# Optimization experiments

Hardware: AMD Instinct MI355X
Metric: run time of the kernel (lower is better)

## Reference

```python
import jax, jax.numpy as jnp
import numpy as np

B, LQ, LK, D, H = 8, 512, 512, 512, 128

def setup_inputs() -> dict:
    key = jax.random.key(0)
    k1, k2, k3, k4, k5 = jax.random.split(key, 5)
    qs = jax.random.normal(k1, (B, LQ, D), dtype=jnp.float32)
    ks = jax.random.normal(k2, (B, LK, D), dtype=jnp.float32)
    # Dense kernels: flax Dense stores kernel as [in_features, out_features]
    Wq = jax.random.normal(k3, (D, H), dtype=jnp.float32) / np.sqrt(D)
    Wk = jax.random.normal(k4, (D, H), dtype=jnp.float32) / np.sqrt(D)
    wv = jax.random.normal(k5, (H,), dtype=jnp.float32) / np.sqrt(H)
    return {"qs": qs, "ks": ks, "Wq": Wq, "Wk": Wk, "wv": wv}

def reference(qs, ks, Wq, Wk, wv):
    # Project queries and keys into the shared hidden space: [B,Lq,H], [B,Lk,H]
    q = jnp.einsum("bqd,dh->bqh", qs, Wq)
    k = jnp.einsum("bkd,dh->bkh", ks, Wk)
    # Broadcast-add -> tanh -> linear reduce over H: scores [B,Lq,Lk]
    feats = jnp.tanh(q[:, :, None, :] + k[:, None, :, :])  # [B,Lq,Lk,H]
    return jnp.einsum("bqkh,h->bqk", feats, wv)
```

## Files before the change

kernel.cpp:

```cpp
#include <hip/hip_runtime.h>
#include <hip/hip_bf16.h>
#include <cstdint>

#define B_   8
#define LQ_  512
#define LK_  512
#define D_   512
#define H_   128

typedef __attribute__((ext_vector_type(8))) short  short8;
typedef __attribute__((ext_vector_type(4))) float  float4v;

#define TANH_C 2.8853900817779268f

__device__ __forceinline__ short bf16rne(float x) {
  uint32_t u = __float_as_uint(x);
  return (short)((u + 0x7fffu + ((u >> 16) & 1u)) >> 16);
}

__device__ __forceinline__ float4v splat4(float x) {
  return (float4v){x, x, x, x};
}

__global__ __launch_bounds__(256) void prep_kernel(
    const float* __restrict__ Wq, const float* __restrict__ Wk,
    const float* __restrict__ wv,
    short* __restrict__ WqF, short* __restrict__ WkF,
    float* __restrict__ w2, float* __restrict__ W0buf) {
  int g = blockIdx.x * 256 + threadIdx.x;
  if (blockIdx.x == 0) {
    int t = threadIdx.x;
    if (t < H_) w2[t] = -2.0f * wv[t];
    if (t == H_) {
      float s = 0.f;
      for (int h = 0; h < H_; ++h) s += wv[h];
      W0buf[0] = s;
    }
  }
  int m = g >> 13;
  int r = g & 8191;
  int l  = r & 63;
  int kb = (r >> 6) & 15;
  int nt = r >> 10;
  int col = nt * 16 + (l & 15);
  int k0  = kb * 32 + ((l >> 4) << 3);
  const float* W = m ? Wk : Wq;
  short8 f;
#pragma unroll
  for (int j = 0; j < 8; ++j) f[j] = bf16rne(W[(k0 + j) * H_ + col]);
  ((short8*)(m ? WkF : WqF))[r] = f;
}

__global__ __launch_bounds__(256) void proj_kernel(
    const float* __restrict__ qs, const float* __restrict__ ks,
    const short* __restrict__ WqF, const short* __restrict__ WkF,
    float* __restrict__ qp, float* __restrict__ kp) {
  int blk  = blockIdx.x;
  int wave = threadIdx.x >> 6;
  int l    = threadIdx.x & 63;
  int grow = blk * 16;
  int m    = (grow >= 4096) ? 1 : 0;
  int r0   = grow - (m ? 4096 : 0);
  const float*  A  = m ? ks : qs;
  const short8* BF = (const short8*)(m ? WkF : WqF);
  float* out = m ? kp : qp;

  float4v acc[2];
  acc[0] = (float4v){0.f, 0.f, 0.f, 0.f};
  acc[1] = (float4v){0.f, 0.f, 0.f, 0.f};

  int quad = l >> 4;
  int arow = r0 + (l & 15);
  const float* aptr = A + (size_t)arow * D_ + quad * 8;
  int t0 = wave * 2;

#pragma unroll 4
  for (int kb = 0; kb < 16; ++kb) {
    float4v a0 = *(const float4v*)(aptr + kb * 32);
    float4v a1 = *(const float4v*)(aptr + kb * 32 + 4);
    short8 af;
#pragma unroll
    for (int j = 0; j < 4; ++j) { af[j] = bf16rne(a0[j]); af[j + 4] = bf16rne(a1[j]); }
#pragma unroll
    for (int tt = 0; tt < 2; ++tt) {
      short8 bf = BF[((t0 + tt) * 16 + kb) * 64 + l];
      acc[tt] = __builtin_amdgcn_mfma_f32_16x16x32_bf16(af, bf, acc[tt], 0, 0, 0);
    }
  }

#pragma unroll
  for (int tt = 0; tt < 2; ++tt)
#pragma unroll
    for (int r = 0; r < 4; ++r) {
      int row = r0 + quad * 4 + r;
      int col = (t0 + tt) * 16 + (l & 15);
      out[(size_t)row * H_ + col] = __builtin_amdgcn_exp2f(acc[tt][r] * TANH_C);
    }
}

__global__ __launch_bounds__(128, 2) void score_kernel(
    const float* __restrict__ qp, const float* __restrict__ kp,
    const float* __restrict__ w2, const float* __restrict__ W0buf,
    float* __restrict__ out) {
  __shared__ float qt[64 * 68];
  __shared__ float kt[64 * 36];
  __shared__ float wl[H_];

  int b = blockIdx.z, qtile = blockIdx.y, ktile = blockIdx.x;
  int t = threadIdx.x;
  int tx = t & 7, ty = t >> 3;

  const float* qbase = qp + (size_t)(b * LQ_ + qtile * 64) * H_;
  const float* kbase = kp + (size_t)(b * LK_ + ktile * 32) * H_;

  float W0 = W0buf[0];

  if (t < 32) *(float4v*)&wl[t * 4] = *(const float4v*)&w2[t * 4];

  float4v acc[4];
  const float4v ones = (float4v){1.f, 1.f, 1.f, 1.f};
#pragma unroll
  for (int i = 0; i < 4; ++i) acc[i] = (float4v){0.f, 0.f, 0.f, 0.f};

  int lr = t >> 4, lc = t & 15;

  for (int hc = 0; hc < 2; ++hc) {
    __syncthreads();
#pragma unroll
    for (int s = 0; s < 8; ++s) {
      int row = lr + 8 * s;
      *(float4v*)&qt[row * 68 + lc * 4] =
          *(const float4v*)&qbase[row * H_ + hc * 64 + lc * 4];
    }
#pragma unroll
    for (int s = 0; s < 4; ++s) {
      int row = lr + 8 * s;
      float4v g = *(const float4v*)&kbase[row * H_ + hc * 64 + lc * 4];
#pragma unroll
      for (int u = 0; u < 4; ++u) kt[(lc * 4 + u) * 36 + row] = g[u];
    }
    __syncthreads();

#pragma unroll 4
    for (int h0 = 0; h0 < 64; h0 += 4) {
      float4v kv[4];
#pragma unroll
      for (int hh = 0; hh < 4; ++hh)
        kv[hh] = *(const float4v*)&kt[(h0 + hh) * 36 + tx * 4];
      float4v w4 = *(const float4v*)&wl[hc * 64 + h0];

#pragma unroll
      for (int i = 0; i < 4; ++i) {
        float4v qv = *(const float4v*)&qt[(ty + 16 * i) * 68 + h0];
        float4v den0 = __builtin_elementwise_fma(splat4(qv[0]), kv[0], ones);
        float4v den1 = __builtin_elementwise_fma(splat4(qv[1]), kv[1], ones);
        float4v den2 = __builtin_elementwise_fma(splat4(qv[2]), kv[2], ones);
        float4v den3 = __builtin_elementwise_fma(splat4(qv[3]), kv[3], ones);
        float4v d01 = den0 * den1;
        float4v d23 = den2 * den3;
        float4v P   = d01 * d23;
        float4v n01 = __builtin_elementwise_fma(splat4(w4[1]), den0, splat4(w4[0]) * den1);
        float4v n23 = __builtin_elementwise_fma(splat4(w4[3]), den2, splat4(w4[2]) * den3);
        float4v N   = __builtin_elementwise_fma(n01, d23, n23 * d01);
        float4v r;
        r[0] = __builtin_amdgcn_rcpf(P[0]);
        r[1] = __builtin_amdgcn_rcpf(P[1]);
        r[2] = __builtin_amdgcn_rcpf(P[2]);
        r[3] = __builtin_amdgcn_rcpf(P[3]);
        acc[i] = __builtin_elementwise_fma(N, r, acc[i]);
      }
    }
  }

  size_t ob = (size_t)(b * LQ_ + qtile * 64) * LK_ + ktile * 32;
#pragma unroll
  for (int i = 0; i < 4; ++i) {
    float4v o = acc[i] + splat4(W0);
    *(float4v*)&out[ob + (size_t)(ty + 16 * i) * LK_ + tx * 4] = o;
  }
}

extern "C" void kernel_launch(void* const* d_in, const int* in_sizes, int n_in,
                              void* d_out, int out_size, void* d_ws, size_t ws_size,
                              hipStream_t stream) {
  const float* qs = (const float*)d_in[0];
  const float* ks = (const float*)d_in[1];
  const float* Wq = (const float*)d_in[2];
  const float* Wk = (const float*)d_in[3];
  const float* wv = (const float*)d_in[4];
  float* out = (float*)d_out;

  char* ws = (char*)d_ws;
  short* WqF  = (short*)ws;
  short* WkF  = (short*)(ws + (128 << 10));
  float* qp   = (float*)(ws + (256 << 10));
  float* kp   = (float*)(ws + (256 << 10) + (2 << 20));
  float* w2   = (float*)(ws + (256 << 10) + (4 << 20));
  float* W0b  = (float*)(ws + (256 << 10) + (4 << 20) + 512);

  prep_kernel<<<64, 256, 0, stream>>>(Wq, Wk, wv, WqF, WkF, w2, W0b);
  proj_kernel<<<512, 256, 0, stream>>>(qs, ks, WqF, WkF, qp, kp);
  score_kernel<<<dim3(16, 8, 8), 128, 0, stream>>>(qp, kp, w2, W0b, out);
}
```

Before: 110.6 us.

## Store key projections transposed and read them directly from global memory in score kernel

```diff
diff --git a/kernel.cpp b/kernel.cpp
--- a/kernel.cpp
+++ b/kernel.cpp
@@ -7,6 +7,7 @@
 #define LK_  512
 #define D_   512
 #define H_   128
+#define NK_  (B_ * LK_)
 
 typedef __attribute__((ext_vector_type(8))) short  short8;
 typedef __attribute__((ext_vector_type(4))) float  float4v;
@@ -54,7 +55,7 @@
 __global__ __launch_bounds__(256) void proj_kernel(
     const float* __restrict__ qs, const float* __restrict__ ks,
     const short* __restrict__ WqF, const short* __restrict__ WkF,
-    float* __restrict__ qp, float* __restrict__ kp) {
+    float* __restrict__ qp, float* __restrict__ kpT) {
   int blk  = blockIdx.x;
   int wave = threadIdx.x >> 6;
   int l    = threadIdx.x & 63;
@@ -63,7 +64,6 @@
   int r0   = grow - (m ? 4096 : 0);
   const float*  A  = m ? ks : qs;
   const short8* BF = (const short8*)(m ? WkF : WqF);
-  float* out = m ? kp : qp;
 
   float4v acc[2];
   acc[0] = (float4v){0.f, 0.f, 0.f, 0.f};
@@ -94,16 +94,17 @@
     for (int r = 0; r < 4; ++r) {
       int row = r0 + quad * 4 + r;
       int col = (t0 + tt) * 16 + (l & 15);
-      out[(size_t)row * H_ + col] = __builtin_amdgcn_exp2f(acc[tt][r] * TANH_C);
+      float e = __builtin_amdgcn_exp2f(acc[tt][r] * TANH_C);
+      if (m) kpT[(size_t)col * NK_ + row] = e;
+      else   qp [(size_t)row * H_  + col] = e;
     }
 }
 
 __global__ __launch_bounds__(128, 2) void score_kernel(
-    const float* __restrict__ qp, const float* __restrict__ kp,
+    const float* __restrict__ qp, const float* __restrict__ kpT,
     const float* __restrict__ w2, const float* __restrict__ W0buf,
     float* __restrict__ out) {
-  __shared__ float qt[64 * 68];
-  __shared__ float kt[64 * 36];
+  __shared__ float qt[64 * 132];
   __shared__ float wl[H_];
 
   int b = blockIdx.z, qtile = blockIdx.y, ktile = blockIdx.x;
@@ -111,7 +112,7 @@
   int tx = t & 7, ty = t >> 3;
 
   const float* qbase = qp + (size_t)(b * LQ_ + qtile * 64) * H_;
-  const float* kbase = kp + (size_t)(b * LK_ + ktile * 32) * H_;
+  const float* kTb   = kpT + (size_t)(b * LK_ + ktile * 32) + tx * 4;
 
   float W0 = W0buf[0];
 
@@ -122,53 +123,41 @@
 #pragma unroll
   for (int i = 0; i < 4; ++i) acc[i] = (float4v){0.f, 0.f, 0.f, 0.f};
 
-  int lr = t >> 4, lc = t & 15;
-
-  for (int hc = 0; hc < 2; ++hc) {
-    __syncthreads();
 #pragma unroll
-    for (int s = 0; s < 8; ++s) {
-      int row = lr + 8 * s;
-      *(float4v*)&qt[row * 68 + lc * 4] =
-          *(const float4v*)&qbase[row * H_ + hc * 64 + lc * 4];
-    }
-#pragma unroll
-    for (int s = 0; s < 4; ++s) {
-      int row = lr + 8 * s;
-      float4v g = *(const float4v*)&kbase[row * H_ + hc * 64 + lc * 4];
-#pragma unroll
-      for (int u = 0; u < 4; ++u) kt[(lc * 4 + u) * 36 + row] = g[u];
-    }
-    __syncthreads();
+  for (int s = 0; s < 16; ++s) {
+    int idx = s * 128 + t;
+    int row = idx >> 5, c4 = idx & 31;
+    *(float4v*)&qt[row * 132 + c4 * 4] = *(const float4v*)&qbase[row * H_ + c4 * 4];
+  }
+  __syncthreads();
 
 #pragma unroll 4
-    for (int h0 = 0; h0 < 64; h0 += 4) {
-      float4v kv[4];
+  for (int h0 = 0; h0 < H_; h0 += 4) {
+    float4v kv[4];
 #pragma unroll
-      for (int hh = 0; hh < 4; ++hh)
-        kv[hh] = *(const float4v*)&kt[(h0 + hh) * 36 + tx * 4];
-      float4v w4 = *(const float4v*)&wl[hc * 64 + h0];
+    for (int hh = 0; hh < 4; ++hh)
+      kv[hh] = *(const float4v*)&kTb[(size_t)(h0 + hh) * NK_];
+    float4v w4 = *(const float4v*)&wl[h0];
 
 #pragma unroll
-      for (int i = 0; i < 4; ++i) {
-        float4v qv = *(const float4v*)&qt[(ty + 16 * i) * 68 + h0];
-        float4v den0 = __builtin_elementwise_fma(splat4(qv[0]), kv[0], ones);
-        float4v den1 = __builtin_elementwise_fma(splat4(qv[1]), kv[1], ones);
-        float4v den2 = __builtin_elementwise_fma(splat4(qv[2]), kv[2], ones);
-        float4v den3 = __builtin_elementwise_fma(splat4(qv[3]), kv[3], ones);
-        float4v d01 = den0 * den1;
-        float4v d23 = den2 * den3;
-        float4v P   = d01 * d23;
-        float4v n01 = __builtin_elementwise_fma(splat4(w4[1]), den0, splat4(w4[0]) * den1);
-        float4v n23 = __builtin_elementwise_fma(splat4(w4[3]), den2, splat4(w4[2]) * den3);
-        float4v N   = __builtin_elementwise_fma(n01, d23, n23 * d01);
-        float4v r;
-        r[0] = __builtin_amdgcn_rcpf(P[0]);
-        r[1] = __builtin_amdgcn_rcpf(P[1]);
-        r[2] = __builtin_amdgcn_rcpf(P[2]);
-        r[3] = __builtin_amdgcn_rcpf(P[3]);
-        acc[i] = __builtin_elementwise_fma(N, r, acc[i]);
-      }
+    for (int i = 0; i < 4; ++i) {
+      float4v qv = *(const float4v*)&qt[(ty + 16 * i) * 132 + h0];
+      float4v den0 = __builtin_elementwise_fma(splat4(qv[0]), kv[0], ones);
+      float4v den1 = __builtin_elementwise_fma(splat4(qv[1]), kv[1], ones);
+      float4v den2 = __builtin_elementwise_fma(splat4(qv[2]), kv[2], ones);
+      float4v den3 = __builtin_elementwise_fma(splat4(qv[3]), kv[3], ones);
+      float4v d01 = den0 * den1;
+      float4v d23 = den2 * den3;
+      float4v P   = d01 * d23;
+      float4v n01 = __builtin_elementwise_fma(splat4(w4[1]), den0, splat4(w4[0]) * den1);
+      float4v n23 = __builtin_elementwise_fma(splat4(w4[3]), den2, splat4(w4[2]) * den3);
+      float4v N   = __builtin_elementwise_fma(n01, d23, n23 * d01);
+      float4v r;
+      r[0] = __builtin_amdgcn_rcpf(P[0]);
+      r[1] = __builtin_amdgcn_rcpf(P[1]);
+      r[2] = __builtin_amdgcn_rcpf(P[2]);
+      r[3] = __builtin_amdgcn_rcpf(P[3]);
+      acc[i] = __builtin_elementwise_fma(N, r, acc[i]);
     }
   }
 
@@ -194,11 +183,11 @@
   short* WqF  = (short*)ws;
   short* WkF  = (short*)(ws + (128 << 10));
   float* qp   = (float*)(ws + (256 << 10));
-  float* kp   = (float*)(ws + (256 << 10) + (2 << 20));
+  float* kpT  = (float*)(ws + (256 << 10) + (2 << 20));
   float* w2   = (float*)(ws + (256 << 10) + (4 << 20));
   float* W0b  = (float*)(ws + (256 << 10) + (4 << 20) + 512);
 
   prep_kernel<<<64, 256, 0, stream>>>(Wq, Wk, wv, WqF, WkF, w2, W0b);
-  proj_kernel<<<512, 256, 0, stream>>>(qs, ks, WqF, WkF, qp, kp);
-  score_kernel<<<dim3(16, 8, 8), 128, 0, stream>>>(qp, kp, w2, W0b, out);
+  proj_kernel<<<512, 256, 0, stream>>>(qs, ks, WqF, WkF, qp, kpT);
+  score_kernel<<<dim3(16, 8, 8), 128, 0, stream>>>(qp, kpT, w2, W0b, out);
 }
```

New measurement: 121.0 us. +9.4%, slower.
